# Kernel optimization log

Measured on AMD Instinct MI355X. Metric: run time of the kernel, lower is better.

Reference implementation:

```python
import jax, jax.numpy as jnp
import numpy as np

N_NODES = 100000
D_IN = 128
D_OUT = 128
N_EDGES = 1600000
BATCH = 500000
LN_EPS = 1e-5


def setup_inputs() -> dict:
    key = jax.random.key(0)
    ks = jax.random.split(key, 9)
    stdv = 1.0 / np.sqrt(D_OUT)
    return {
        "x": jax.random.randint(ks[0], (BATCH,), 0, N_NODES + 1, dtype=jnp.int64)
             if jax.config.jax_enable_x64 else jax.random.randint(ks[0], (BATCH,), 0, N_NODES + 1, dtype=jnp.int32),
        "embeddings": jax.random.normal(ks[1], (N_NODES, D_IN), dtype=jnp.float32),
        "weight": jax.random.uniform(ks[2], (D_IN, D_OUT), minval=-stdv, maxval=stdv, dtype=jnp.float32),
        "bias": jax.random.uniform(ks[3], (D_OUT,), minval=-stdv, maxval=stdv, dtype=jnp.float32),
        "vals": jax.random.uniform(ks[4], (N_EDGES,), dtype=jnp.float32),
        "rows": jax.random.randint(ks[5], (N_EDGES,), 0, N_NODES, dtype=jnp.int32),
        "cols": jax.random.randint(ks[6], (N_EDGES,), 0, N_NODES, dtype=jnp.int32),
        "gamma": jnp.ones((D_OUT,), dtype=jnp.float32),
        "beta": jnp.zeros((D_OUT,), dtype=jnp.float32),
    }


def reference(x, embeddings, weight, bias, vals, rows, cols, gamma, beta):
    n = embeddings.shape[0]
    # Conv_layer: dense linear + sparse adjacency matmul (SpMM via gather + segment_sum)
    h = embeddings @ weight + bias                       # [N, D_OUT]
    msg = vals[:, None] * h[cols]                        # [E, D_OUT]
    h = jax.ops.segment_sum(msg, rows, num_segments=n)   # [N, D_OUT]
    # relu then LayerNorm
    h = jax.nn.relu(h)
    mu = jnp.mean(h, axis=-1, keepdims=True)
    var = jnp.mean(jnp.square(h - mu), axis=-1, keepdims=True)
    h = (h - mu) * jax.lax.rsqrt(var + LN_EPS) * gamma + beta
    # masked gather into output table: valid indices are in [1, N]
    select = (x >= 1) & (x < n + 1)
    idx = jnp.clip(x - 1, 0, n - 1)
    final = jnp.where(select[:, None], h[idx, :], 0.0)   # [B, D_OUT]
    return final
```

## Files before the change

### kernel.cpp

```cpp
#include <hip/hip_runtime.h>
#include <hip/hip_bf16.h>

#define D 128

typedef __attribute__((ext_vector_type(8))) short s8v;
typedef __attribute__((ext_vector_type(4))) float f4v;

__device__ inline unsigned short bf16rne(float f) {
  unsigned u = __float_as_uint(f);
  u += 0x7fff + ((u >> 16) & 1);
  return (unsigned short)(u >> 16);
}
__device__ inline float bf2f(unsigned short h) {
  return __uint_as_float(((unsigned)h) << 16);
}

__global__ __launch_bounds__(256) void wconv(
    const float* __restrict__ W, unsigned short* __restrict__ WT16) {
  int idx = blockIdx.x * 256 + threadIdx.x;
  int k = idx >> 7, n = idx & 127;
  WT16[n * 128 + k] = bf16rne(W[idx]);
}

__global__ __launch_bounds__(256) void gemm_hist(
    const float* __restrict__ emb, const unsigned short* __restrict__ WT16,
    const float* __restrict__ bias, unsigned short* __restrict__ A16,
    int nNodes, int gemmBlocks,
    const int* __restrict__ rows, int* __restrict__ cnt, int nEdges) {
  if ((int)blockIdx.x >= gemmBlocks) {
    int e = ((int)blockIdx.x - gemmBlocks) * 256 + threadIdx.x;
    if (e < nEdges) atomicAdd(&cnt[rows[e]], 1);
    return;
  }
  const int tid = threadIdx.x;
  const int w = tid >> 6;
  const int lane = tid & 63;
  const int m = lane & 15;
  const int kb = lane >> 4;
  const int r0 = (int)blockIdx.x * 64 + w * 16;
  int rowA = r0 + m;
  if (rowA > nNodes - 1) rowA = nNodes - 1;
  const float* arow = emb + (size_t)rowA * D + kb * 8;

  f4v acc[8];
#pragma unroll
  for (int t = 0; t < 8; ++t) acc[t] = (f4v){0.f, 0.f, 0.f, 0.f};

#pragma unroll
  for (int ks = 0; ks < 4; ++ks) {
    const int k0 = ks * 32;
    float4 a0 = *(const float4*)(arow + k0);
    float4 a1 = *(const float4*)(arow + k0 + 4);
    s8v af;
    af[0] = (short)bf16rne(a0.x); af[1] = (short)bf16rne(a0.y);
    af[2] = (short)bf16rne(a0.z); af[3] = (short)bf16rne(a0.w);
    af[4] = (short)bf16rne(a1.x); af[5] = (short)bf16rne(a1.y);
    af[6] = (short)bf16rne(a1.z); af[7] = (short)bf16rne(a1.w);
#pragma unroll
    for (int nt = 0; nt < 8; ++nt) {
      int n = nt * 16 + m;
      s8v bf = *(const s8v*)&WT16[n * 128 + k0 + kb * 8];
      acc[nt] = __builtin_amdgcn_mfma_f32_16x16x32_bf16(af, bf, acc[nt], 0, 0, 0);
    }
  }

#pragma unroll
  for (int nt = 0; nt < 8; ++nt) {
    int col = nt * 16 + m;
    float bcol = bias[col];
#pragma unroll
    for (int reg = 0; reg < 4; ++reg) {
      int row = r0 + kb * 4 + reg;
      if (row < nNodes)
        A16[(size_t)row * D + col] = bf16rne(acc[nt][reg] + bcol);
    }
  }
}

__global__ __launch_bounds__(1024) void scan_local(
    const int* __restrict__ cnt, int* __restrict__ start,
    int* __restrict__ bsum, int n) {
  __shared__ int wsum[16];
  __shared__ int wpre[16];
  const int tid = threadIdx.x;
  const int lane = tid & 63;
  const int wid = tid >> 6;
  int i = blockIdx.x * 1024 + tid;
  int v = (i < n) ? cnt[i] : 0;
  int inc = v;
#pragma unroll
  for (int st = 1; st < 64; st <<= 1) {
    int t = __shfl_up(inc, st);
    if (lane >= st) inc += t;
  }
  if (lane == 63) wsum[wid] = inc;
  __syncthreads();
  if (tid < 16) {
    int wv = wsum[tid];
    int winc = wv;
#pragma unroll
    for (int st = 1; st < 16; st <<= 1) {
      int t = __shfl_up(winc, st);
      if (lane >= st) winc += t;
    }
    wpre[tid] = winc - wv;
    if (tid == 15) bsum[blockIdx.x] = winc;
  }
  __syncthreads();
  if (i < n) start[i] = inc - v + wpre[wid];
}

__global__ __launch_bounds__(1024) void scan_top(int* __restrict__ bsum, int nb) {
  __shared__ int wsum[16];
  __shared__ int wpre[16];
  const int tid = threadIdx.x;
  const int lane = tid & 63;
  const int wid = tid >> 6;
  int v = (tid < nb) ? bsum[tid] : 0;
  int inc = v;
#pragma unroll
  for (int st = 1; st < 64; st <<= 1) {
    int t = __shfl_up(inc, st);
    if (lane >= st) inc += t;
  }
  if (lane == 63) wsum[wid] = inc;
  __syncthreads();
  if (tid < 16) {
    int wv = wsum[tid];
    int winc = wv;
#pragma unroll
    for (int st = 1; st < 16; st <<= 1) {
      int t = __shfl_up(winc, st);
      if (lane >= st) winc += t;
    }
    wpre[tid] = winc - wv;
  }
  __syncthreads();
  if (tid < nb) bsum[tid] = inc - v + wpre[wid];
}

__global__ __launch_bounds__(1024) void scan_add(
    int* __restrict__ start, const int* __restrict__ bsum,
    int* __restrict__ cursor, int n, int nCur) {
  int i = blockIdx.x * 1024 + threadIdx.x;
  if (i < n) {
    int s = start[i] + bsum[blockIdx.x];
    start[i] = s;
    if (i < nCur) cursor[i] = s;
  }
}

__global__ __launch_bounds__(256) void scatter_build(
    const int* __restrict__ rows, const int* __restrict__ cols,
    const float* __restrict__ vals, int* __restrict__ cursor,
    int2* __restrict__ edata, int nEdges) {
  int e = blockIdx.x * 256 + threadIdx.x;
  if (e >= nEdges) return;
  int r = rows[e];
  int p = atomicAdd(&cursor[r], 1);
  int2 cv;
  cv.x = cols[e];
  cv.y = __float_as_int(vals[e]);
  edata[p] = cv;
}

__global__ __launch_bounds__(256) void segsum_relu_ln(
    const unsigned short* __restrict__ A16, const int2* __restrict__ edata,
    const int* __restrict__ start, const float* __restrict__ gamma,
    const float* __restrict__ beta, unsigned short* __restrict__ H16, int nNodes) {
  int node = blockIdx.x * 4 + (threadIdx.x >> 6);
  if (node >= nNodes) return;
  const int lane = threadIdx.x & 63;
  const int g = lane >> 4;
  const int li = lane & 15;
  int p = start[node];
  const int pend = start[node + 1];

  float acc[8];
#pragma unroll
  for (int j = 0; j < 8; ++j) acc[j] = 0.f;

  for (; p < pend; p += 8) {
    int p0 = p + g;
    int p1 = p + 4 + g;
    int2 cv0 = make_int2(0, 0);
    int2 cv1 = make_int2(0, 0);
    if (p0 < pend) cv0 = edata[p0];
    if (p1 < pend) cv1 = edata[p1];
    float v0 = __int_as_float(cv0.y);
    float v1 = __int_as_float(cv1.y);
    uint4 u0 = ((const uint4*)(A16 + (size_t)cv0.x * D))[li];
    uint4 u1 = ((const uint4*)(A16 + (size_t)cv1.x * D))[li];
    acc[0] += v0 * bf2f((unsigned short)(u0.x & 0xffff));
    acc[1] += v0 * bf2f((unsigned short)(u0.x >> 16));
    acc[2] += v0 * bf2f((unsigned short)(u0.y & 0xffff));
    acc[3] += v0 * bf2f((unsigned short)(u0.y >> 16));
    acc[4] += v0 * bf2f((unsigned short)(u0.z & 0xffff));
    acc[5] += v0 * bf2f((unsigned short)(u0.z >> 16));
    acc[6] += v0 * bf2f((unsigned short)(u0.w & 0xffff));
    acc[7] += v0 * bf2f((unsigned short)(u0.w >> 16));
    acc[0] += v1 * bf2f((unsigned short)(u1.x & 0xffff));
    acc[1] += v1 * bf2f((unsigned short)(u1.x >> 16));
    acc[2] += v1 * bf2f((unsigned short)(u1.y & 0xffff));
    acc[3] += v1 * bf2f((unsigned short)(u1.y >> 16));
    acc[4] += v1 * bf2f((unsigned short)(u1.z & 0xffff));
    acc[5] += v1 * bf2f((unsigned short)(u1.z >> 16));
    acc[6] += v1 * bf2f((unsigned short)(u1.w & 0xffff));
    acc[7] += v1 * bf2f((unsigned short)(u1.w >> 16));
  }
#pragma unroll
  for (int j = 0; j < 8; ++j) {
    acc[j] += __shfl_xor(acc[j], 16);
    acc[j] += __shfl_xor(acc[j], 32);
  }
  float s = 0.f, sq = 0.f;
#pragma unroll
  for (int j = 0; j < 8; ++j) {
    acc[j] = fmaxf(acc[j], 0.f);
    s += acc[j];
    sq += acc[j] * acc[j];
  }
#pragma unroll
  for (int off = 8; off >= 1; off >>= 1) {
    s += __shfl_xor(s, off);
    sq += __shfl_xor(sq, off);
  }
  float mean = s * (1.f / 128.f);
  float var = sq * (1.f / 128.f) - mean * mean;
  float rstd = rsqrtf(var + 1e-5f);

  float4 g0 = ((const float4*)gamma)[li * 2];
  float4 g1 = ((const float4*)gamma)[li * 2 + 1];
  float4 b0 = ((const float4*)beta)[li * 2];
  float4 b1 = ((const float4*)beta)[li * 2 + 1];
  if (g == 0) {
    unsigned o0 = bf16rne((acc[0] - mean) * rstd * g0.x + b0.x)
                | ((unsigned)bf16rne((acc[1] - mean) * rstd * g0.y + b0.y) << 16);
    unsigned o1 = bf16rne((acc[2] - mean) * rstd * g0.z + b0.z)
                | ((unsigned)bf16rne((acc[3] - mean) * rstd * g0.w + b0.w) << 16);
    unsigned o2 = bf16rne((acc[4] - mean) * rstd * g1.x + b1.x)
                | ((unsigned)bf16rne((acc[5] - mean) * rstd * g1.y + b1.y) << 16);
    unsigned o3 = bf16rne((acc[6] - mean) * rstd * g1.z + b1.z)
                | ((unsigned)bf16rne((acc[7] - mean) * rstd * g1.w + b1.w) << 16);
    uint4 o = make_uint4(o0, o1, o2, o3);
    ((uint4*)(H16 + (size_t)node * D))[li] = o;
  }
}

__global__ __launch_bounds__(256) void gather_out(
    const int* __restrict__ x, const unsigned short* __restrict__ H16,
    float* __restrict__ out, int batch, int nNodes) {
  long gid = (long)blockIdx.x * 256 + threadIdx.x;
  int b = (int)(gid >> 4);
  int j = (int)(gid & 15);
  if (b >= batch) return;
  int xv = x[b];
  f4v r0 = (f4v){0.f, 0.f, 0.f, 0.f};
  f4v r1 = (f4v){0.f, 0.f, 0.f, 0.f};
  if (xv >= 1 && xv <= nNodes) {
    uint4 u = ((const uint4*)(H16 + (size_t)(xv - 1) * D))[j];
    r0 = (f4v){bf2f((unsigned short)(u.x & 0xffff)), bf2f((unsigned short)(u.x >> 16)),
               bf2f((unsigned short)(u.y & 0xffff)), bf2f((unsigned short)(u.y >> 16))};
    r1 = (f4v){bf2f((unsigned short)(u.z & 0xffff)), bf2f((unsigned short)(u.z >> 16)),
               bf2f((unsigned short)(u.w & 0xffff)), bf2f((unsigned short)(u.w >> 16))};
  }
  f4v* o = (f4v*)out + gid * 2;
  __builtin_nontemporal_store(r0, o);
  __builtin_nontemporal_store(r1, o + 1);
}

extern "C" void kernel_launch(void* const* d_in, const int* in_sizes, int n_in,
                              void* d_out, int out_size, void* d_ws, size_t ws_size,
                              hipStream_t stream) {
  const int* x = (const int*)d_in[0];
  const float* emb = (const float*)d_in[1];
  const float* W = (const float*)d_in[2];
  const float* bias = (const float*)d_in[3];
  const float* vals = (const float*)d_in[4];
  const int* rows = (const int*)d_in[5];
  const int* cols = (const int*)d_in[6];
  const float* gamma = (const float*)d_in[7];
  const float* beta = (const float*)d_in[8];
  float* out = (float*)d_out;

  const int batch = in_sizes[0];
  const int nNodes = in_sizes[1] / D;
  const int nEdges = in_sizes[4];
  const int n1 = nNodes + 1;
  const int nb = (n1 + 1023) / 1024;

  const size_t tab16 = (((size_t)nNodes * D * 2 + 255) / 256) * 256;
  const size_t cntB = (((size_t)n1 * 4 + 255) / 256) * 256;
  const size_t curB = (((size_t)nNodes * 4 + 255) / 256) * 256;
  const size_t bsB = (((size_t)nb * 4 + 255) / 256) * 256;
  const size_t wtB = (size_t)128 * 128 * 2;

  uint8_t* p = (uint8_t*)d_ws;
  unsigned short* A16 = (unsigned short*)p; p += tab16;
  unsigned short* H16 = (unsigned short*)p; p += tab16;
  unsigned short* WT16 = (unsigned short*)p; p += wtB;
  int* cnt = (int*)p; p += cntB;
  int* start = (int*)p; p += cntB;
  int* cursor = (int*)p; p += curB;
  int* bsum = (int*)p; p += bsB;
  int2* edata = (int2*)p;

  const int gemmBlocks = (nNodes + 63) / 64;
  const int histBlocks = (nEdges + 255) / 256;

  hipMemsetAsync(cnt, 0, (size_t)n1 * sizeof(int), stream);
  wconv<<<64, 256, 0, stream>>>(W, WT16);
  gemm_hist<<<gemmBlocks + histBlocks, 256, 0, stream>>>(
      emb, WT16, bias, A16, nNodes, gemmBlocks, rows, cnt, nEdges);
  scan_local<<<nb, 1024, 0, stream>>>(cnt, start, bsum, n1);
  scan_top<<<1, 1024, 0, stream>>>(bsum, nb);
  scan_add<<<nb, 1024, 0, stream>>>(start, bsum, cursor, n1, nNodes);
  scatter_build<<<(nEdges + 255) / 256, 256, 0, stream>>>(rows, cols, vals, cursor, edata, nEdges);
  segsum_relu_ln<<<(nNodes + 3) / 4, 256, 0, stream>>>(A16, edata, start, gamma, beta, H16, nNodes);
  long gthreads = (long)batch * 16;
  gather_out<<<(int)((gthreads + 255) / 256), 256, 0, stream>>>(x, H16, out, batch, nNodes);
}
```

Baseline: 605.6 us.

## Fuse memset into weight-convert, drop scan_top, vectorize histogram, unroll segsum by four

```diff
diff --git a/kernel.cpp b/kernel.cpp
--- a/kernel.cpp
+++ b/kernel.cpp
@@ -15,11 +15,22 @@
   return __uint_as_float(((unsigned)h) << 16);
 }
 
-__global__ __launch_bounds__(256) void wconv(
-    const float* __restrict__ W, unsigned short* __restrict__ WT16) {
-  int idx = blockIdx.x * 256 + threadIdx.x;
-  int k = idx >> 7, n = idx & 127;
-  WT16[n * 128 + k] = bf16rne(W[idx]);
+__global__ __launch_bounds__(256) void init_wt_cnt(
+    const float* __restrict__ W, unsigned short* __restrict__ WT16,
+    int* __restrict__ cnt, int n1) {
+  const int b = blockIdx.x;
+  if (b < 64) {
+    int idx = b * 256 + threadIdx.x;
+    int k = idx >> 7, n = idx & 127;
+    WT16[n * 128 + k] = bf16rne(W[idx]);
+  } else {
+    int i = (b - 64) * 1024 + threadIdx.x * 4;
+    if (i + 3 < n1) {
+      *(int4*)(cnt + i) = make_int4(0, 0, 0, 0);
+    } else {
+      for (int j = i; j < n1; ++j) cnt[j] = 0;
+    }
+  }
 }
 
 __global__ __launch_bounds__(256) void gemm_hist(
@@ -28,8 +39,16 @@
     int nNodes, int gemmBlocks,
     const int* __restrict__ rows, int* __restrict__ cnt, int nEdges) {
   if ((int)blockIdx.x >= gemmBlocks) {
-    int e = ((int)blockIdx.x - gemmBlocks) * 256 + threadIdx.x;
-    if (e < nEdges) atomicAdd(&cnt[rows[e]], 1);
+    int base = (((int)blockIdx.x - gemmBlocks) * 256 + threadIdx.x) * 4;
+    if (base + 3 < nEdges) {
+      int4 r = *(const int4*)(rows + base);
+      atomicAdd(&cnt[r.x], 1);
+      atomicAdd(&cnt[r.y], 1);
+      atomicAdd(&cnt[r.z], 1);
+      atomicAdd(&cnt[r.w], 1);
+    } else {
+      for (int e = base; e < nEdges; ++e) atomicAdd(&cnt[rows[e]], 1);
+    }
     return;
   }
   const int tid = threadIdx.x;
@@ -110,41 +129,23 @@
   if (i < n) start[i] = inc - v + wpre[wid];
 }
 
-__global__ __launch_bounds__(1024) void scan_top(int* __restrict__ bsum, int nb) {
-  __shared__ int wsum[16];
-  __shared__ int wpre[16];
-  const int tid = threadIdx.x;
-  const int lane = tid & 63;
-  const int wid = tid >> 6;
-  int v = (tid < nb) ? bsum[tid] : 0;
-  int inc = v;
-#pragma unroll
-  for (int st = 1; st < 64; st <<= 1) {
-    int t = __shfl_up(inc, st);
-    if (lane >= st) inc += t;
-  }
-  if (lane == 63) wsum[wid] = inc;
-  __syncthreads();
-  if (tid < 16) {
-    int wv = wsum[tid];
-    int winc = wv;
-#pragma unroll
-    for (int st = 1; st < 16; st <<= 1) {
-      int t = __shfl_up(winc, st);
-      if (lane >= st) winc += t;
-    }
-    wpre[tid] = winc - wv;
-  }
-  __syncthreads();
-  if (tid < nb) bsum[tid] = inc - v + wpre[wid];
-}
-
 __global__ __launch_bounds__(1024) void scan_add(
     int* __restrict__ start, const int* __restrict__ bsum,
     int* __restrict__ cursor, int n, int nCur) {
-  int i = blockIdx.x * 1024 + threadIdx.x;
+  __shared__ int boff_s;
+  const int tid = threadIdx.x;
+  if (tid < 64) {
+    int ssum = 0;
+    for (int j = tid; j < (int)blockIdx.x; j += 64) ssum += bsum[j];
+#pragma unroll
+    for (int off = 32; off >= 1; off >>= 1) ssum += __shfl_xor(ssum, off);
+    if (tid == 0) boff_s = ssum;
+  }
+  __syncthreads();
+  const int boff = boff_s;
+  int i = blockIdx.x * 1024 + tid;
   if (i < n) {
-    int s = start[i] + bsum[blockIdx.x];
+    int s = start[i] + boff;
     start[i] = s;
     if (i < nCur) cursor[i] = s;
   }
@@ -180,17 +181,22 @@
 #pragma unroll
   for (int j = 0; j < 8; ++j) acc[j] = 0.f;
 
-  for (; p < pend; p += 8) {
-    int p0 = p + g;
-    int p1 = p + 4 + g;
-    int2 cv0 = make_int2(0, 0);
-    int2 cv1 = make_int2(0, 0);
+  for (; p < pend; p += 16) {
+    int2 cv0 = make_int2(0, 0), cv1 = make_int2(0, 0);
+    int2 cv2 = make_int2(0, 0), cv3 = make_int2(0, 0);
+    int p0 = p + g, p1 = p + 4 + g, p2 = p + 8 + g, p3 = p + 12 + g;
     if (p0 < pend) cv0 = edata[p0];
     if (p1 < pend) cv1 = edata[p1];
+    if (p2 < pend) cv2 = edata[p2];
+    if (p3 < pend) cv3 = edata[p3];
+    uint4 u0 = ((const uint4*)(A16 + (size_t)cv0.x * D))[li];
+    uint4 u1 = ((const uint4*)(A16 + (size_t)cv1.x * D))[li];
+    uint4 u2 = ((const uint4*)(A16 + (size_t)cv2.x * D))[li];
+    uint4 u3 = ((const uint4*)(A16 + (size_t)cv3.x * D))[li];
     float v0 = __int_as_float(cv0.y);
     float v1 = __int_as_float(cv1.y);
-    uint4 u0 = ((const uint4*)(A16 + (size_t)cv0.x * D))[li];
-    uint4 u1 = ((const uint4*)(A16 + (size_t)cv1.x * D))[li];
+    float v2 = __int_as_float(cv2.y);
+    float v3 = __int_as_float(cv3.y);
     acc[0] += v0 * bf2f((unsigned short)(u0.x & 0xffff));
     acc[1] += v0 * bf2f((unsigned short)(u0.x >> 16));
     acc[2] += v0 * bf2f((unsigned short)(u0.y & 0xffff));
@@ -207,6 +213,22 @@
     acc[5] += v1 * bf2f((unsigned short)(u1.z >> 16));
     acc[6] += v1 * bf2f((unsigned short)(u1.w & 0xffff));
     acc[7] += v1 * bf2f((unsigned short)(u1.w >> 16));
+    acc[0] += v2 * bf2f((unsigned short)(u2.x & 0xffff));
+    acc[1] += v2 * bf2f((unsigned short)(u2.x >> 16));
+    acc[2] += v2 * bf2f((unsigned short)(u2.y & 0xffff));
+    acc[3] += v2 * bf2f((unsigned short)(u2.y >> 16));
+    acc[4] += v2 * bf2f((unsigned short)(u2.z & 0xffff));
+    acc[5] += v2 * bf2f((unsigned short)(u2.z >> 16));
+    acc[6] += v2 * bf2f((unsigned short)(u2.w & 0xffff));
+    acc[7] += v2 * bf2f((unsigned short)(u2.w >> 16));
+    acc[0] += v3 * bf2f((unsigned short)(u3.x & 0xffff));
+    acc[1] += v3 * bf2f((unsigned short)(u3.x >> 16));
+    acc[2] += v3 * bf2f((unsigned short)(u3.y & 0xffff));
+    acc[3] += v3 * bf2f((unsigned short)(u3.y >> 16));
+    acc[4] += v3 * bf2f((unsigned short)(u3.z & 0xffff));
+    acc[5] += v3 * bf2f((unsigned short)(u3.z >> 16));
+    acc[6] += v3 * bf2f((unsigned short)(u3.w & 0xffff));
+    acc[7] += v3 * bf2f((unsigned short)(u3.w >> 16));
   }
 #pragma unroll
   for (int j = 0; j < 8; ++j) {
@@ -306,14 +328,13 @@
   int2* edata = (int2*)p;
 
   const int gemmBlocks = (nNodes + 63) / 64;
-  const int histBlocks = (nEdges + 255) / 256;
-
-  hipMemsetAsync(cnt, 0, (size_t)n1 * sizeof(int), stream);
-  wconv<<<64, 256, 0, stream>>>(W, WT16);
+  const int histBlocks = (nEdges + 1023) / 1024;
+  const int initBlocks = 64 + (n1 + 1023) / 1024;
+
+  init_wt_cnt<<<initBlocks, 256, 0, stream>>>(W, WT16, cnt, n1);
   gemm_hist<<<gemmBlocks + histBlocks, 256, 0, stream>>>(
       emb, WT16, bias, A16, nNodes, gemmBlocks, rows, cnt, nEdges);
   scan_local<<<nb, 1024, 0, stream>>>(cnt, start, bsum, n1);
-  scan_top<<<1, 1024, 0, stream>>>(bsum, nb);
   scan_add<<<nb, 1024, 0, stream>>>(start, bsum, cursor, n1, nNodes);
   scatter_build<<<(nEdges + 255) / 256, 256, 0, stream>>>(rows, cols, vals, cursor, edata, nEdges);
   segsum_relu_ln<<<(nNodes + 3) / 4, 256, 0, stream>>>(A16, edata, start, gamma, beta, H16, nNodes);
```

Measured after the change: 599.2 us. Within noise of the previous version (-1.1%).
